# Performance work log

Measured on AMD Instinct MI355X. Metric: run time of the kernel, lower is better.

Reference implementation:

```python
import jax, jax.numpy as jnp
import numpy as np

B, U = 64, 512            # batch, max_units
AE = 1024
UE = 256                  # unit_embedding_size
A = 256                   # target_head_attention_size


def setup_inputs() -> dict:
    key = jax.random.key(0)
    ks = jax.random.split(key, 10)
    return {
        "autoregressive_embedding": jax.random.normal(ks[0], (B, U, AE), jnp.float32),
        "own_unit_embeddings": jax.random.normal(ks[1], (B, U, UE), jnp.float32),
        "enemy_unit_embeddings": jax.random.normal(ks[2], (B, U, UE), jnp.float32),
        "nr_own_units": jax.random.randint(ks[3], (B, 1), 0, U).astype(jnp.int64),
        "nr_units_enemy": jax.random.randint(ks[4], (B, 1), 0, U).astype(jnp.int64),
        "nr_own_flags": jax.random.randint(ks[5], (B, 1), 0, 8).astype(jnp.int64),
        "Wq": jax.random.normal(ks[6], (UE + AE, A), jnp.float32) * (1.0 / np.sqrt(UE + AE)),
        "bq": jnp.zeros((A,), jnp.float32),
        "Wk": jax.random.normal(ks[7], (UE, A), jnp.float32) * (1.0 / np.sqrt(UE)),
        "bk": jnp.zeros((A,), jnp.float32),
    }


def reference(autoregressive_embedding, own_unit_embeddings, enemy_unit_embeddings,
              nr_own_units, nr_units_enemy, nr_own_flags, Wq, bq, Wk, bk):
    # combined: [B, U, AE+UE]
    combined = jnp.concatenate([autoregressive_embedding, own_unit_embeddings], axis=2)
    queries = combined @ Wq + bq                       # [B, U, A]
    keys = enemy_unit_embeddings @ Wk + bk             # [B, U, A]
    attention = jnp.einsum("bqd,bkd->bqk", queries, keys) / (A ** 0.5)  # [B, U, U]
    # Vectorized mask: rows in [nr_own_flags, nr_own_units), cols in [0, nr_units_enemy)
    idx = jnp.arange(U)
    row_ok = (idx[None, :] >= nr_own_flags) & (idx[None, :] < nr_own_units)  # [B, U]
    col_ok = idx[None, :] < nr_units_enemy                                   # [B, U]
    mask = jnp.where(row_ok[:, :, None] & col_ok[:, None, :], 1.0, 1e-9)     # [B, U, U]
    return jax.nn.softmax(attention * mask, axis=-1)
```

## Files before the change

kernel.cpp:

```cpp
#include <hip/hip_runtime.h>

constexpr int B  = 64;
constexpr int U  = 512;
constexpr int AE = 1024;
constexpr int UE = 256;
constexpr int A  = 256;
constexpr int KQ = AE + UE;

typedef _Float16 f16x8 __attribute__((ext_vector_type(8)));
typedef float    f32x4 __attribute__((ext_vector_type(4)));

__global__ void prep(const float* __restrict__ Wq, const float* __restrict__ Wk,
                     _Float16* __restrict__ WqT, _Float16* __restrict__ WkT) {
    int idx = blockIdx.x * 256 + threadIdx.x;
    if (idx < KQ * A) {
        int k = idx >> 8, n = idx & 255;
        WqT[(size_t)n * KQ + k] = (_Float16)Wq[idx];
    } else {
        int j = idx - KQ * A;
        if (j < A * A) {
            int k = j >> 8, n = j & 255;
            WkT[(size_t)n * A + k] = (_Float16)Wk[j];
        }
    }
}

__global__ __launch_bounds__(512) void gemm(
    const float* __restrict__ A1, int s1, int split,
    const float* __restrict__ A2, int s2,
    const _Float16* __restrict__ BT,
    const float* __restrict__ bias,
    _Float16* __restrict__ Out,
    int Ktot)
{
    __shared__ __align__(16) _Float16 Al[2][64][32];
    __shared__ __align__(16) _Float16 Bl[2][256][32];

    const int t    = threadIdx.x;
    const int lane = t & 63;
    const int w    = t >> 6;
    const int mbase = blockIdx.x * 64;

    const int wm = (w & 1) * 32;
    const int wn = (w >> 1) * 64;

    f32x4 acc[2][4] = {};

    const int ar  = t >> 3;
    const int aq  = t & 7;
    const int ap  = aq >> 2;
    const int asw = ((aq & 3) ^ ((ar >> 1) & 3)) * 8;
    const size_t grow = mbase + ar;

    int bp[4], bn[4], bq[4], bsw[4];
    #pragma unroll
    for (int j = 0; j < 4; j++) {
        int s = j * 512 + t;
        bp[j] = s >> 10;
        bn[j] = (s & 1023) >> 2;
        bq[j] = s & 3;
        bsw[j] = ((bq[j] ^ ((bn[j] >> 1) & 3))) * 8;
    }

    float4 areg0, areg1;
    f16x8 breg[4];

    auto loadA = [&](int k0) {
        int kg = k0 + aq * 8;
        const float* src = (kg < split) ? (A1 + grow * (size_t)s1 + kg)
                                        : (A2 + grow * (size_t)s2 + (kg - split));
        areg0 = ((const float4*)src)[0];
        areg1 = ((const float4*)src)[1];
    };
    auto loadB = [&](int k0) {
        #pragma unroll
        for (int j = 0; j < 4; j++)
            breg[j] = *(const f16x8*)(BT + (size_t)bn[j] * Ktot + k0 + bp[j] * 32 + bq[j] * 8);
    };

    loadA(0);
    loadB(0);

    const int rsw = (((lane & 15) >> 1) & 3);
    const int nk = Ktot >> 6;
    for (int kb = 0; kb < nk; kb++) {
        __syncthreads();
        {
            f16x8 hv;
            hv[0] = (_Float16)areg0.x; hv[1] = (_Float16)areg0.y;
            hv[2] = (_Float16)areg0.z; hv[3] = (_Float16)areg0.w;
            hv[4] = (_Float16)areg1.x; hv[5] = (_Float16)areg1.y;
            hv[6] = (_Float16)areg1.z; hv[7] = (_Float16)areg1.w;
            *(f16x8*)(&Al[ap][ar][asw]) = hv;
            #pragma unroll
            for (int j = 0; j < 4; j++)
                *(f16x8*)(&Bl[bp[j]][bn[j]][bsw[j]]) = breg[j];
        }
        __syncthreads();
        if (kb + 1 < nk) { loadA(kb * 64 + 64); loadB(kb * 64 + 64); }
        #pragma unroll
        for (int p = 0; p < 2; p++) {
            f16x8 af[2], bf[4];
            #pragma unroll
            for (int mt = 0; mt < 2; mt++)
                af[mt] = *(const f16x8*)(&Al[p][wm + mt * 16 + (lane & 15)][(((lane >> 4) ^ rsw)) * 8]);
            #pragma unroll
            for (int nt = 0; nt < 4; nt++)
                bf[nt] = *(const f16x8*)(&Bl[p][wn + nt * 16 + (lane & 15)][(((lane >> 4) ^ rsw)) * 8]);
            #pragma unroll
            for (int mt = 0; mt < 2; mt++)
                #pragma unroll
                for (int nt = 0; nt < 4; nt++)
                    acc[mt][nt] = __builtin_amdgcn_mfma_f32_16x16x32_f16(
                        af[mt], bf[nt], acc[mt][nt], 0, 0, 0);
        }
    }
    const int col0 = wn + (lane & 15);
    const int rsub = (lane >> 4) * 4;
    #pragma unroll
    for (int nt = 0; nt < 4; nt++) {
        const int col = col0 + nt * 16;
        const float bv = bias[col];
        const int c5 = col >> 5, c31 = col & 31;
        #pragma unroll
        for (int mt = 0; mt < 2; mt++)
            #pragma unroll
            for (int r = 0; r < 4; r++) {
                int row = mbase + wm + mt * 16 + rsub + r;
                int bb = row >> 9, u = row & 511;
                Out[(((size_t)bb * 8 + c5) * 512 + u) * 32 + c31] =
                    (_Float16)(acc[mt][nt][r] + bv);
            }
    }
}

__global__ __launch_bounds__(512) void attn(
    const _Float16* __restrict__ Qh, const _Float16* __restrict__ Kh,
    const int* __restrict__ nr_own_units, const int* __restrict__ nr_units_enemy,
    const int* __restrict__ nr_own_flags, float* __restrict__ Out)
{
    __shared__ __align__(16) _Float16 Ql[8][64][32];
    __shared__ __align__(16) _Float16 Kl[512][32];
    __shared__ float red[64][4];

    const int t    = threadIdx.x;
    const int lane = t & 63;
    const int w    = t >> 6;
    const int b    = blockIdx.y;
    const int qbase = blockIdx.x * 64;

    const int nf = nr_own_flags[b];
    const int nu = nr_own_units[b];
    const int ne = nr_units_enemy[b];

    const int wm = (w & 1) * 32;
    const int wn = (w >> 1) * 128;

    f16x8 qreg[4];
    {
        const _Float16* Qb = Qh + ((size_t)b * 8 * 512 + qbase) * 32;
        #pragma unroll
        for (int j = 0; j < 4; j++) {
            int s = j * 512 + t;
            int p = s >> 8, row = (s & 255) >> 2, cq = s & 3;
            qreg[j] = *(const f16x8*)(Qb + ((size_t)p * 512 + row) * 32 + cq * 8);
        }
        #pragma unroll
        for (int j = 0; j < 4; j++) {
            int s = j * 512 + t;
            int p = s >> 8, row = (s & 255) >> 2, cq = s & 3;
            *(f16x8*)(&Ql[p][row][(cq ^ ((row >> 1) & 3)) * 8]) = qreg[j];
        }
    }

    const _Float16* Kb = Kh + (size_t)b * 8 * 512 * 32;
    f16x8 kreg[4];
    const int krow = t >> 2;
    const int kq   = t & 3;
    auto loadK = [&](int c) {
        const _Float16* Kc = Kb + (size_t)c * 512 * 32;
        #pragma unroll
        for (int j = 0; j < 4; j++)
            kreg[j] = *(const f16x8*)(Kc + ((size_t)(j * 128 + krow)) * 32 + kq * 8);
    };
    loadK(0);

    f32x4 acc[2][8] = {};
    const int rsw = (((lane & 15) >> 1) & 3);
    for (int c = 0; c < 8; c++) {
        __syncthreads();
        #pragma unroll
        for (int j = 0; j < 4; j++) {
            int row = j * 128 + krow;
            *(f16x8*)(&Kl[row][(kq ^ ((row >> 1) & 3)) * 8]) = kreg[j];
        }
        __syncthreads();
        if (c < 7) loadK(c + 1);
        f16x8 af[2], bf[8];
        #pragma unroll
        for (int mt = 0; mt < 2; mt++)
            af[mt] = *(const f16x8*)(&Ql[c][wm + mt * 16 + (lane & 15)][((lane >> 4) ^ rsw) * 8]);
        #pragma unroll
        for (int nt = 0; nt < 8; nt++)
            bf[nt] = *(const f16x8*)(&Kl[wn + nt * 16 + (lane & 15)][((lane >> 4) ^ rsw) * 8]);
        #pragma unroll
        for (int mt = 0; mt < 2; mt++)
            #pragma unroll
            for (int nt = 0; nt < 8; nt++)
                acc[mt][nt] = __builtin_amdgcn_mfma_f32_16x16x32_f16(
                    af[mt], bf[nt], acc[mt][nt], 0, 0, 0);
    }

    const int rsub = (lane >> 4) * 4;
    #pragma unroll
    for (int mt = 0; mt < 2; mt++)
        #pragma unroll
        for (int nt = 0; nt < 8; nt++)
            #pragma unroll
            for (int r = 0; r < 4; r++) {
                int rl = wm + mt * 16 + rsub + r;
                int uq = qbase + rl;
                int col = wn + nt * 16 + (lane & 15);
                bool ok = (col < ne) && (uq >= nf) && (uq < nu);
                acc[mt][nt][r] = acc[mt][nt][r] * 0.0625f * (ok ? 1.0f : 1e-9f);
            }

    float mx[2][4];
    #pragma unroll
    for (int mt = 0; mt < 2; mt++)
        #pragma unroll
        for (int r = 0; r < 4; r++) {
            float m = acc[mt][0][r];
            #pragma unroll
            for (int nt = 1; nt < 8; nt++) m = fmaxf(m, acc[mt][nt][r]);
            #pragma unroll
            for (int off = 1; off <= 8; off <<= 1) m = fmaxf(m, __shfl_xor(m, off));
            mx[mt][r] = m;
        }
    if ((lane & 15) == 0) {
        #pragma unroll
        for (int mt = 0; mt < 2; mt++)
            #pragma unroll
            for (int r = 0; r < 4; r++)
                red[wm + mt * 16 + rsub + r][w >> 1] = mx[mt][r];
    }
    __syncthreads();
    #pragma unroll
    for (int mt = 0; mt < 2; mt++)
        #pragma unroll
        for (int r = 0; r < 4; r++) {
            f32x4 v = *(const f32x4*)(&red[wm + mt * 16 + rsub + r][0]);
            mx[mt][r] = fmaxf(fmaxf(v[0], v[1]), fmaxf(v[2], v[3]));
        }
    __syncthreads();

    float sm[2][4];
    #pragma unroll
    for (int mt = 0; mt < 2; mt++)
        #pragma unroll
        for (int r = 0; r < 4; r++) {
            float s = 0.f;
            #pragma unroll
            for (int nt = 0; nt < 8; nt++) {
                float e = __expf(acc[mt][nt][r] - mx[mt][r]);
                acc[mt][nt][r] = e;
                s += e;
            }
            #pragma unroll
            for (int off = 1; off <= 8; off <<= 1) s += __shfl_xor(s, off);
            sm[mt][r] = s;
        }
    if ((lane & 15) == 0) {
        #pragma unroll
        for (int mt = 0; mt < 2; mt++)
            #pragma unroll
            for (int r = 0; r < 4; r++)
                red[wm + mt * 16 + rsub + r][w >> 1] = sm[mt][r];
    }
    __syncthreads();

    #pragma unroll
    for (int mt = 0; mt < 2; mt++)
        #pragma unroll
        for (int r = 0; r < 4; r++) {
            int rl = wm + mt * 16 + rsub + r;
            f32x4 v = *(const f32x4*)(&red[rl][0]);
            float inv = 1.0f / (v[0] + v[1] + v[2] + v[3]);
            float* orow = Out + ((size_t)b * 512 + qbase + rl) * 512 + wn + (lane & 15);
            #pragma unroll
            for (int nt = 0; nt < 8; nt++)
                orow[nt * 16] = acc[mt][nt][r] * inv;
        }
}

extern "C" void kernel_launch(void* const* d_in, const int* in_sizes, int n_in,
                              void* d_out, int out_size, void* d_ws, size_t ws_size,
                              hipStream_t stream) {
    const float* ar    = (const float*)d_in[0];
    const float* own   = (const float*)d_in[1];
    const float* enemy = (const float*)d_in[2];
    const int*   n_own   = (const int*)d_in[3];
    const int*   n_enemy = (const int*)d_in[4];
    const int*   n_flags = (const int*)d_in[5];
    const float* Wq = (const float*)d_in[6];
    const float* bq = (const float*)d_in[7];
    const float* Wk = (const float*)d_in[8];
    const float* bk = (const float*)d_in[9];
    float* out = (float*)d_out;

    char* ws = (char*)d_ws;
    _Float16* WqT = (_Float16*)(ws);
    _Float16* WkT = (_Float16*)(ws + 655360);
    _Float16* Qh  = (_Float16*)(ws + 786432);
    _Float16* Kh  = (_Float16*)(ws + 786432 + 16777216);

    prep<<<dim3((KQ * A + A * A) / 256), dim3(256), 0, stream>>>(Wq, Wk, WqT, WkT);

    gemm<<<dim3(512), dim3(512), 0, stream>>>(ar, AE, AE, own, UE, WqT, bq, Qh, KQ);
    gemm<<<dim3(512), dim3(512), 0, stream>>>(enemy, UE, 0, enemy, UE, WkT, bk, Kh, A);

    attn<<<dim3(8, B), dim3(512), 0, stream>>>(Qh, Kh, n_own, n_enemy, n_flags, out);
}
```

Before: 331.4 us.

## Drop LDS staging in gemm and attn; load MFMA fragments directly from global

Both the projection GEMM and the attention kernel stop staging tiles through shared memory. Each wave now loads its MFMA A/B fragments straight from global memory, with 256-thread blocks, larger per-wave N tiles and no barriers in the K loop. The attention kernel also halves its query tile to 32 rows, doubling the grid. This removes LDS writes and syncs but makes each wave issue redundant global loads that rely on L2/L1 for reuse, with less coalesced access.

```diff
diff --git a/kernel.cpp b/kernel.cpp
--- a/kernel.cpp
+++ b/kernel.cpp
@@ -25,7 +25,7 @@
     }
 }
 
-__global__ __launch_bounds__(512) void gemm(
+__global__ __launch_bounds__(256, 2) void gemm(
     const float* __restrict__ A1, int s1, int split,
     const float* __restrict__ A2, int s2,
     const _Float16* __restrict__ BT,
@@ -33,100 +33,59 @@
     _Float16* __restrict__ Out,
     int Ktot)
 {
-    __shared__ __align__(16) _Float16 Al[2][64][32];
-    __shared__ __align__(16) _Float16 Bl[2][256][32];
-
     const int t    = threadIdx.x;
     const int lane = t & 63;
     const int w    = t >> 6;
-    const int mbase = blockIdx.x * 64;
-
-    const int wm = (w & 1) * 32;
-    const int wn = (w >> 1) * 64;
-
-    f32x4 acc[2][4] = {};
-
-    const int ar  = t >> 3;
-    const int aq  = t & 7;
-    const int ap  = aq >> 2;
-    const int asw = ((aq & 3) ^ ((ar >> 1) & 3)) * 8;
-    const size_t grow = mbase + ar;
-
-    int bp[4], bn[4], bq[4], bsw[4];
-    #pragma unroll
-    for (int j = 0; j < 4; j++) {
-        int s = j * 512 + t;
-        bp[j] = s >> 10;
-        bn[j] = (s & 1023) >> 2;
-        bq[j] = s & 3;
-        bsw[j] = ((bq[j] ^ ((bn[j] >> 1) & 3))) * 8;
-    }
-
-    float4 areg0, areg1;
-    f16x8 breg[4];
-
-    auto loadA = [&](int k0) {
-        int kg = k0 + aq * 8;
-        const float* src = (kg < split) ? (A1 + grow * (size_t)s1 + kg)
-                                        : (A2 + grow * (size_t)s2 + (kg - split));
-        areg0 = ((const float4*)src)[0];
-        areg1 = ((const float4*)src)[1];
-    };
-    auto loadB = [&](int k0) {
-        #pragma unroll
-        for (int j = 0; j < 4; j++)
-            breg[j] = *(const f16x8*)(BT + (size_t)bn[j] * Ktot + k0 + bp[j] * 32 + bq[j] * 8);
-    };
-
-    loadA(0);
-    loadB(0);
-
-    const int rsw = (((lane & 15) >> 1) & 3);
-    const int nk = Ktot >> 6;
-    for (int kb = 0; kb < nk; kb++) {
-        __syncthreads();
-        {
+    const int lm   = lane & 15;
+    const int lk   = (lane >> 4) * 8;
+    const int wm   = blockIdx.x * 64 + (w & 1) * 32;
+    const int wn   = (w >> 1) * 128;
+
+    f32x4 acc[2][8] = {};
+
+    const size_t r0 = wm + lm;
+    const size_t r1 = wm + 16 + lm;
+
+    #pragma unroll 2
+    for (int k0 = 0; k0 < Ktot; k0 += 32) {
+        const int kg = k0 + lk;
+        f16x8 af[2], bf[8];
+        #pragma unroll
+        for (int mt = 0; mt < 2; mt++) {
+            const size_t row = mt ? r1 : r0;
+            const float* src = (kg < split) ? (A1 + row * (size_t)s1 + kg)
+                                            : (A2 + row * (size_t)s2 + (kg - split));
+            const float4 x = ((const float4*)src)[0];
+            const float4 y = ((const float4*)src)[1];
             f16x8 hv;
-            hv[0] = (_Float16)areg0.x; hv[1] = (_Float16)areg0.y;
-            hv[2] = (_Float16)areg0.z; hv[3] = (_Float16)areg0.w;
-            hv[4] = (_Float16)areg1.x; hv[5] = (_Float16)areg1.y;
-            hv[6] = (_Float16)areg1.z; hv[7] = (_Float16)areg1.w;
-            *(f16x8*)(&Al[ap][ar][asw]) = hv;
-            #pragma unroll
-            for (int j = 0; j < 4; j++)
-                *(f16x8*)(&Bl[bp[j]][bn[j]][bsw[j]]) = breg[j];
-        }
-        __syncthreads();
-        if (kb + 1 < nk) { loadA(kb * 64 + 64); loadB(kb * 64 + 64); }
-        #pragma unroll
-        for (int p = 0; p < 2; p++) {
-            f16x8 af[2], bf[4];
-            #pragma unroll
-            for (int mt = 0; mt < 2; mt++)
-                af[mt] = *(const f16x8*)(&Al[p][wm + mt * 16 + (lane & 15)][(((lane >> 4) ^ rsw)) * 8]);
-            #pragma unroll
-            for (int nt = 0; nt < 4; nt++)
-                bf[nt] = *(const f16x8*)(&Bl[p][wn + nt * 16 + (lane & 15)][(((lane >> 4) ^ rsw)) * 8]);
-            #pragma unroll
-            for (int mt = 0; mt < 2; mt++)
-                #pragma unroll
-                for (int nt = 0; nt < 4; nt++)
-                    acc[mt][nt] = __builtin_amdgcn_mfma_f32_16x16x32_f16(
-                        af[mt], bf[nt], acc[mt][nt], 0, 0, 0);
-        }
-    }
-    const int col0 = wn + (lane & 15);
+            hv[0] = (_Float16)x.x; hv[1] = (_Float16)x.y;
+            hv[2] = (_Float16)x.z; hv[3] = (_Float16)x.w;
+            hv[4] = (_Float16)y.x; hv[5] = (_Float16)y.y;
+            hv[6] = (_Float16)y.z; hv[7] = (_Float16)y.w;
+            af[mt] = hv;
+        }
+        #pragma unroll
+        for (int nt = 0; nt < 8; nt++)
+            bf[nt] = *(const f16x8*)(BT + (size_t)(wn + nt * 16 + lm) * Ktot + kg);
+        #pragma unroll
+        for (int mt = 0; mt < 2; mt++)
+            #pragma unroll
+            for (int nt = 0; nt < 8; nt++)
+                acc[mt][nt] = __builtin_amdgcn_mfma_f32_16x16x32_f16(
+                    af[mt], bf[nt], acc[mt][nt], 0, 0, 0);
+    }
+
     const int rsub = (lane >> 4) * 4;
     #pragma unroll
-    for (int nt = 0; nt < 4; nt++) {
-        const int col = col0 + nt * 16;
+    for (int nt = 0; nt < 8; nt++) {
+        const int col = wn + nt * 16 + lm;
         const float bv = bias[col];
         const int c5 = col >> 5, c31 = col & 31;
         #pragma unroll
         for (int mt = 0; mt < 2; mt++)
             #pragma unroll
             for (int r = 0; r < 4; r++) {
-                int row = mbase + wm + mt * 16 + rsub + r;
+                int row = wm + mt * 16 + rsub + r;
                 int bb = row >> 9, u = row & 511;
                 Out[(((size_t)bb * 8 + c5) * 512 + u) * 32 + c31] =
                     (_Float16)(acc[mt][nt][r] + bv);
@@ -134,81 +93,46 @@
     }
 }
 
-__global__ __launch_bounds__(512) void attn(
+__global__ __launch_bounds__(256, 2) void attn(
     const _Float16* __restrict__ Qh, const _Float16* __restrict__ Kh,
     const int* __restrict__ nr_own_units, const int* __restrict__ nr_units_enemy,
     const int* __restrict__ nr_own_flags, float* __restrict__ Out)
 {
-    __shared__ __align__(16) _Float16 Ql[8][64][32];
-    __shared__ __align__(16) _Float16 Kl[512][32];
-    __shared__ float red[64][4];
+    __shared__ float red[32][4];
 
     const int t    = threadIdx.x;
     const int lane = t & 63;
     const int w    = t >> 6;
+    const int lm   = lane & 15;
+    const int lk   = (lane >> 4) * 8;
     const int b    = blockIdx.y;
-    const int qbase = blockIdx.x * 64;
+    const int qbase = blockIdx.x * 32;
+    const int wn   = w * 128;
 
     const int nf = nr_own_flags[b];
     const int nu = nr_own_units[b];
     const int ne = nr_units_enemy[b];
 
-    const int wm = (w & 1) * 32;
-    const int wn = (w >> 1) * 128;
-
-    f16x8 qreg[4];
-    {
-        const _Float16* Qb = Qh + ((size_t)b * 8 * 512 + qbase) * 32;
-        #pragma unroll
-        for (int j = 0; j < 4; j++) {
-            int s = j * 512 + t;
-            int p = s >> 8, row = (s & 255) >> 2, cq = s & 3;
-            qreg[j] = *(const f16x8*)(Qb + ((size_t)p * 512 + row) * 32 + cq * 8);
-        }
-        #pragma unroll
-        for (int j = 0; j < 4; j++) {
-            int s = j * 512 + t;
-            int p = s >> 8, row = (s & 255) >> 2, cq = s & 3;
-            *(f16x8*)(&Ql[p][row][(cq ^ ((row >> 1) & 3)) * 8]) = qreg[j];
-        }
-    }
-
+    const _Float16* Qb = Qh + (size_t)b * 8 * 512 * 32;
     const _Float16* Kb = Kh + (size_t)b * 8 * 512 * 32;
-    f16x8 kreg[4];
-    const int krow = t >> 2;
-    const int kq   = t & 3;
-    auto loadK = [&](int c) {
-        const _Float16* Kc = Kb + (size_t)c * 512 * 32;
-        #pragma unroll
-        for (int j = 0; j < 4; j++)
-            kreg[j] = *(const f16x8*)(Kc + ((size_t)(j * 128 + krow)) * 32 + kq * 8);
-    };
-    loadK(0);
 
     f32x4 acc[2][8] = {};
-    const int rsw = (((lane & 15) >> 1) & 3);
+
+    #pragma unroll 2
     for (int c = 0; c < 8; c++) {
-        __syncthreads();
-        #pragma unroll
-        for (int j = 0; j < 4; j++) {
-            int row = j * 128 + krow;
-            *(f16x8*)(&Kl[row][(kq ^ ((row >> 1) & 3)) * 8]) = kreg[j];
-        }
-        __syncthreads();
-        if (c < 7) loadK(c + 1);
-        f16x8 af[2], bf[8];
-        #pragma unroll
-        for (int mt = 0; mt < 2; mt++)
-            af[mt] = *(const f16x8*)(&Ql[c][wm + mt * 16 + (lane & 15)][((lane >> 4) ^ rsw) * 8]);
+        f16x8 qf[2], bf[8];
+        #pragma unroll
+        for (int mt = 0; mt < 2; mt++)
+            qf[mt] = *(const f16x8*)(Qb + ((size_t)c * 512 + qbase + mt * 16 + lm) * 32 + lk);
         #pragma unroll
         for (int nt = 0; nt < 8; nt++)
-            bf[nt] = *(const f16x8*)(&Kl[wn + nt * 16 + (lane & 15)][((lane >> 4) ^ rsw) * 8]);
+            bf[nt] = *(const f16x8*)(Kb + ((size_t)c * 512 + wn + nt * 16 + lm) * 32 + lk);
         #pragma unroll
         for (int mt = 0; mt < 2; mt++)
             #pragma unroll
             for (int nt = 0; nt < 8; nt++)
                 acc[mt][nt] = __builtin_amdgcn_mfma_f32_16x16x32_f16(
-                    af[mt], bf[nt], acc[mt][nt], 0, 0, 0);
+                    qf[mt], bf[nt], acc[mt][nt], 0, 0, 0);
     }
 
     const int rsub = (lane >> 4) * 4;
@@ -218,9 +142,8 @@
         for (int nt = 0; nt < 8; nt++)
             #pragma unroll
             for (int r = 0; r < 4; r++) {
-                int rl = wm + mt * 16 + rsub + r;
-                int uq = qbase + rl;
-                int col = wn + nt * 16 + (lane & 15);
+                int uq = qbase + mt * 16 + rsub + r;
+                int col = wn + nt * 16 + lm;
                 bool ok = (col < ne) && (uq >= nf) && (uq < nu);
                 acc[mt][nt][r] = acc[mt][nt][r] * 0.0625f * (ok ? 1.0f : 1e-9f);
             }
@@ -237,19 +160,19 @@
             for (int off = 1; off <= 8; off <<= 1) m = fmaxf(m, __shfl_xor(m, off));
             mx[mt][r] = m;
         }
-    if ((lane & 15) == 0) {
+    if (lm == 0) {
         #pragma unroll
         for (int mt = 0; mt < 2; mt++)
             #pragma unroll
             for (int r = 0; r < 4; r++)
-                red[wm + mt * 16 + rsub + r][w >> 1] = mx[mt][r];
+                red[mt * 16 + rsub + r][w] = mx[mt][r];
     }
     __syncthreads();
     #pragma unroll
     for (int mt = 0; mt < 2; mt++)
         #pragma unroll
         for (int r = 0; r < 4; r++) {
-            f32x4 v = *(const f32x4*)(&red[wm + mt * 16 + rsub + r][0]);
+            f32x4 v = *(const f32x4*)(&red[mt * 16 + rsub + r][0]);
             mx[mt][r] = fmaxf(fmaxf(v[0], v[1]), fmaxf(v[2], v[3]));
         }
     __syncthreads();
@@ -270,12 +193,12 @@
             for (int off = 1; off <= 8; off <<= 1) s += __shfl_xor(s, off);
             sm[mt][r] = s;
         }
-    if ((lane & 15) == 0) {
+    if (lm == 0) {
         #pragma unroll
         for (int mt = 0; mt < 2; mt++)
             #pragma unroll
             for (int r = 0; r < 4; r++)
-                red[wm + mt * 16 + rsub + r][w >> 1] = sm[mt][r];
+                red[mt * 16 + rsub + r][w] = sm[mt][r];
     }
     __syncthreads();
 
@@ -283,10 +206,10 @@
     for (int mt = 0; mt < 2; mt++)
         #pragma unroll
         for (int r = 0; r < 4; r++) {
-            int rl = wm + mt * 16 + rsub + r;
+            int rl = mt * 16 + rsub + r;
             f32x4 v = *(const f32x4*)(&red[rl][0]);
             float inv = 1.0f / (v[0] + v[1] + v[2] + v[3]);
-            float* orow = Out + ((size_t)b * 512 + qbase + rl) * 512 + wn + (lane & 15);
+            float* orow = Out + ((size_t)b * 512 + qbase + rl) * 512 + wn + lm;
             #pragma unroll
             for (int nt = 0; nt < 8; nt++)
                 orow[nt * 16] = acc[mt][nt][r] * inv;
@@ -316,8 +239,8 @@
 
     prep<<<dim3((KQ * A + A * A) / 256), dim3(256), 0, stream>>>(Wq, Wk, WqT, WkT);
 
-    gemm<<<dim3(512), dim3(512), 0, stream>>>(ar, AE, AE, own, UE, WqT, bq, Qh, KQ);
-    gemm<<<dim3(512), dim3(512), 0, stream>>>(enemy, UE, 0, enemy, UE, WkT, bk, Kh, A);
-
-    attn<<<dim3(8, B), dim3(512), 0, stream>>>(Qh, Kh, n_own, n_enemy, n_flags, out);
-}
+    gemm<<<dim3(512), dim3(256), 0, stream>>>(ar, AE, AE, own, UE, WqT, bq, Qh, KQ);
+    gemm<<<dim3(512), dim3(256), 0, stream>>>(enemy, UE, 0, enemy, UE, WkT, bk, Kh, A);
+
+    attn<<<dim3(16, B), dim3(256), 0, stream>>>(Qh, Kh, n_own, n_enemy, n_flags, out);
+}
```

Result: slower. 409.8 us (+23.7%).
